# Optimization experiments

Hardware: AMD Instinct MI355X
Metric: run time of the kernel (lower is better)

## Reference

```python
import jax, jax.numpy as jnp
import numpy as np

S_SCALE = 64.0   # arcface scale
MARGIN = 0.5     # arcface additive angular margin
EMB = 512
NUM_CLASSES = 100000
BATCH = 512


def setup_inputs() -> dict:
    key = jax.random.key(0)
    k1, k2, k3, k4 = jax.random.split(key, 4)
    # xavier_uniform for [num_classes, emb]
    limit = float(np.sqrt(6.0 / (NUM_CLASSES + EMB)))
    weight = jax.random.uniform(k1, (NUM_CLASSES, EMB), jnp.float32, -limit, limit)
    fc_weight = jax.random.uniform(k2, (NUM_CLASSES, EMB), jnp.float32, -limit, limit)
    local_embeddings = jax.random.normal(k3, (BATCH, EMB), jnp.float32)
    local_labels = jax.random.randint(k4, (BATCH,), 0, NUM_CLASSES, jnp.int64)
    return {
        "local_embeddings": local_embeddings,
        "weight": weight,
        "fc_weight": fc_weight,
        "local_labels": local_labels,
        "epoch": 40,
    }


def _l2norm(x, eps=1e-12):
    return x / jnp.maximum(jnp.linalg.norm(x, axis=-1, keepdims=True), eps)


def _arcface(logits, labels):
    # insightface ArcFace: replace target cosine with cos(theta + m), then scale by s
    rows = jnp.arange(logits.shape[0])
    target = logits[rows, labels]
    sin = jnp.sqrt(jnp.maximum(1.0 - target * target, 0.0))
    cos_m, sin_m = jnp.cos(MARGIN), jnp.sin(MARGIN)
    with_margin = target * cos_m - sin * sin_m            # cos(theta + m)
    # safeguard: only apply when theta + m <= pi  (target > cos(pi - m))
    threshold = jnp.cos(jnp.pi - MARGIN)
    mm = jnp.sin(jnp.pi - MARGIN) * MARGIN
    new_target = jnp.where(target > threshold, with_margin, target - mm)
    logits = logits.at[rows, labels].set(new_target)
    return logits * S_SCALE


def _ce(logits, labels):
    rows = jnp.arange(logits.shape[0])
    logp = jax.nn.log_softmax(logits, axis=-1)
    return -jnp.mean(logp[rows, labels])


def reference(local_embeddings, weight, fc_weight, local_labels, epoch):
    labels = local_labels.astype(jnp.int32)
    # margin branch: normalize both sides, cosine logits, arcface margin, CE
    norm_emb = _l2norm(local_embeddings)
    norm_w = _l2norm(weight)
    logits = norm_emb @ norm_w.T                   # [B, num_classes]
    logits = _arcface(logits, labels)
    margin_loss = _ce(logits, labels)
    # plain CE branch on raw linear
    ce_logits = local_embeddings @ fc_weight.T     # [B, num_classes]
    ce_loss = _ce(ce_logits, labels)
    if epoch <= 30:
        return ce_loss + 0.0 * margin_loss
    else:
        return 0.0 * ce_loss + margin_loss
```

## Files before the change

kernel.cpp:

```cpp
#include <hip/hip_runtime.h>

typedef float floatx4 __attribute__((ext_vector_type(4)));
typedef int   intx4   __attribute__((ext_vector_type(4)));
typedef int   intx8   __attribute__((ext_vector_type(8)));

#define NC      100000
#define EMBD    512
#define BATCH   512
#define BN      64
#define NCH     1563
#define NGB     196

#define COS_M   0.8775825618903728f
#define SIN_M   0.479425538604203f
#define THRESH  (-0.8775825618903728f)
#define MM_C    0.2397127693021015f

__device__ __forceinline__ uint2 pack8_fp8(float4 a, float4 b) {
  int lo = 0, hi = 0;
  lo = __builtin_amdgcn_cvt_pk_fp8_f32(a.x, a.y, lo, false);
  lo = __builtin_amdgcn_cvt_pk_fp8_f32(a.z, a.w, lo, true);
  hi = __builtin_amdgcn_cvt_pk_fp8_f32(b.x, b.y, hi, false);
  hi = __builtin_amdgcn_cvt_pk_fp8_f32(b.z, b.w, hi, true);
  return make_uint2((unsigned)lo, (unsigned)hi);
}

__global__ __launch_bounds__(256) void prep_small_k(
    const float* __restrict__ emb, const float* __restrict__ weight,
    const float* __restrict__ fcw, const int* __restrict__ labels,
    const int* __restrict__ epoch, unsigned char* __restrict__ Aq,
    float* __restrict__ tsc, int* __restrict__ lab32,
    float* __restrict__ out) {
  const bool mm = (*epoch > 30);
  const int tid = threadIdx.x;
  const int pred = (labels[2 * tid + 1] != 0) ? 1 : 0;
  const bool is64 = (__syncthreads_or(pred) == 0);

  const int w = tid >> 6, lane = tid & 63;
  const int row = blockIdx.x * 4 + w;
  const int lab = is64 ? labels[2 * row] : labels[row];
  const float* W = mm ? weight : fcw;

  const float* er = emb + (size_t)row * EMBD + lane * 8;
  const float* wr = W + (size_t)lab * EMBD + lane * 8;
  float4 e0 = *(const float4*)er,  e1 = *(const float4*)(er + 4);
  float4 w0 = *(const float4*)wr,  w1 = *(const float4*)(wr + 4);
  float dot = e0.x*w0.x + e0.y*w0.y + e0.z*w0.z + e0.w*w0.w
            + e1.x*w1.x + e1.y*w1.y + e1.z*w1.z + e1.w*w1.w;
  float ssa = e0.x*e0.x + e0.y*e0.y + e0.z*e0.z + e0.w*e0.w
            + e1.x*e1.x + e1.y*e1.y + e1.z*e1.z + e1.w*e1.w;
  float ssw = w0.x*w0.x + w0.y*w0.y + w0.z*w0.z + w0.w*w0.w
            + w1.x*w1.x + w1.y*w1.y + w1.z*w1.z + w1.w*w1.w;
  #pragma unroll
  for (int off = 32; off; off >>= 1) {
    dot += __shfl_xor(dot, off, 64);
    ssa += __shfl_xor(ssa, off, 64);
    ssw += __shfl_xor(ssw, off, 64);
  }
  const float inva = mm ? (1.0f / fmaxf(sqrtf(ssa), 1e-12f)) : 1.0f;
  float4 q0 = make_float4(e0.x*inva, e0.y*inva, e0.z*inva, e0.w*inva);
  float4 q1 = make_float4(e1.x*inva, e1.y*inva, e1.z*inva, e1.w*inva);
  *(uint2*)(Aq + (size_t)row * EMBD + lane * 8) = pack8_fp8(q0, q1);

  if (lane == 0) {
    lab32[row] = lab;
    float tv;
    if (mm) {
      float cosv = dot / (fmaxf(sqrtf(ssa), 1e-12f) * fmaxf(sqrtf(ssw), 1e-12f));
      float sinv = sqrtf(fmaxf(1.0f - cosv * cosv, 0.0f));
      float wmarg = cosv * COS_M - sinv * SIN_M;
      float nt = (cosv > THRESH) ? wmarg : (cosv - MM_C);
      tv = 64.0f * nt;
    } else {
      tv = dot;
    }
    tsc[row] = tv;
  }
  if (blockIdx.x == 0 && tid == 0) out[0] = 0.0f;
}

__global__ __launch_bounds__(256, 2) void gemm_fused_k(
    const unsigned char* __restrict__ Aq, const float* __restrict__ weight,
    const float* __restrict__ fcw, const float* __restrict__ tsc,
    const int* __restrict__ lab32, const int* __restrict__ epoch,
    float2* __restrict__ partials) {
  const int t = blockIdx.x & 31, gblk = blockIdx.x >> 5;
  const int bn = gblk * 8 + (t & 7);
  const int bm = t >> 3;
  if (bn >= NCH) return;

  const bool mm = (*epoch > 30);
  const float scale = mm ? 64.0f : 1.0f;
  const float* __restrict__ Wp = mm ? weight : fcw;

  __shared__ unsigned char Bs[BN * EMBD];
  __shared__ float tscS[128];
  __shared__ int   labS[128];

  const int tid  = threadIdx.x;
  const int lane = tid & 63;
  const int w    = tid >> 6;
  const int m0   = bm * 128;
  const int n0   = bn * BN;

  if (tid < 128) { tscS[tid] = tsc[m0 + tid]; labS[tid] = lab32[m0 + tid]; }

  #pragma unroll 4
  for (int rr = 0; rr < 16; ++rr) {
    const int r    = w * 16 + rr;
    const int grow = n0 + r;
    uint2 pq = make_uint2(0u, 0u);
    if (grow < NC) {
      const float* src = Wp + (size_t)grow * EMBD + lane * 8;
      float4 a = *(const float4*)src;
      float4 b = *(const float4*)(src + 4);
      float ss = a.x*a.x + a.y*a.y + a.z*a.z + a.w*a.w
               + b.x*b.x + b.y*b.y + b.z*b.z + b.w*b.w;
      #pragma unroll
      for (int off = 32; off; off >>= 1) ss += __shfl_xor(ss, off, 64);
      const float inv = mm ? (1.0f / fmaxf(sqrtf(ss), 1e-12f)) : 1.0f;
      float4 qa = make_float4(a.x*inv, a.y*inv, a.z*inv, a.w*inv);
      float4 qb = make_float4(b.x*inv, b.y*inv, b.z*inv, b.w*inv);
      pq = pack8_fp8(qa, qb);
    }
    const int addr = r * EMBD + ((lane >> 4) << 7)
                   + (((((lane >> 1) & 7) ^ (r & 7))) << 4) + ((lane & 1) << 3);
    *(uint2*)&Bs[addr] = pq;
  }
  __syncthreads();

  const int rsel = lane & 15;
  const int g32  = (lane >> 4) * 32;
  const int c0   = ((((lane >> 4) * 2)     ^ (rsel & 7)) << 4);
  const int c1   = (((((lane >> 4) * 2)+1) ^ (rsel & 7)) << 4);

  floatx4 acc[2][4];
  #pragma unroll
  for (int i = 0; i < 2; i++)
    #pragma unroll
    for (int j = 0; j < 4; j++) acc[i][j] = (floatx4){0.f, 0.f, 0.f, 0.f};

  #pragma unroll
  for (int kt = 0; kt < 4; ++kt) {
    intx8 af[2];
    #pragma unroll
    for (int mi = 0; mi < 2; mi++) {
      const unsigned char* ap =
          Aq + (size_t)(m0 + w * 32 + mi * 16 + rsel) * EMBD + kt * 128 + g32;
      intx4 alo = *(const intx4*)ap;
      intx4 ahi = *(const intx4*)(ap + 16);
      af[mi] = __builtin_shufflevector(alo, ahi, 0, 1, 2, 3, 4, 5, 6, 7);
    }
    intx8 bv[4];
    #pragma unroll
    for (int ni = 0; ni < 4; ni++) {
      const int base = (ni * 16 + rsel) * EMBD + kt * 128;
      intx4 lo = *(const intx4*)&Bs[base + c0];
      intx4 hi = *(const intx4*)&Bs[base + c1];
      bv[ni] = __builtin_shufflevector(lo, hi, 0, 1, 2, 3, 4, 5, 6, 7);
    }
    #pragma unroll
    for (int mi = 0; mi < 2; mi++)
      #pragma unroll
      for (int ni = 0; ni < 4; ni++)
        acc[mi][ni] = __builtin_amdgcn_mfma_scale_f32_16x16x128_f8f6f4(
            af[mi], bv[ni], acc[mi][ni], 0, 0,
            0, 0x7f7f7f7f, 0, 0x7f7f7f7f);
  }

  const int colq = lane & 15;
  #pragma unroll
  for (int mi = 0; mi < 2; mi++) {
    #pragma unroll
    for (int r = 0; r < 4; r++) {
      const int rl = w * 32 + mi * 16 + (lane >> 4) * 4 + r;
      const int lab = labS[rl];
      const float tv = tscS[rl];
      float v[4];
      #pragma unroll
      for (int ni = 0; ni < 4; ni++) {
        const int cg = n0 + ni * 16 + colq;
        float x = acc[mi][ni][r] * scale;
        if (cg >= NC) x = -1e30f;
        else if (cg == lab) x = tv;
        v[ni] = x;
      }
      float mx = v[0];
      #pragma unroll
      for (int ni = 1; ni < 4; ni++) mx = fmaxf(mx, v[ni]);
      #pragma unroll
      for (int off = 1; off < 16; off <<= 1) mx = fmaxf(mx, __shfl_xor(mx, off, 64));
      float s = 0.0f;
      #pragma unroll
      for (int ni = 0; ni < 4; ni++) s += __expf(v[ni] - mx);
      #pragma unroll
      for (int off = 1; off < 16; off <<= 1) s += __shfl_xor(s, off, 64);
      if (colq == 0)
        partials[(size_t)(m0 + rl) * NCH + bn] = make_float2(mx, s);
    }
  }
}

__global__ __launch_bounds__(256) void rowmerge_k(
    const float2* __restrict__ partials, const float* __restrict__ tsc,
    float* __restrict__ out) {
  const int row = blockIdx.x;
  const int tid = threadIdx.x;
  float M = -1e30f, S = 0.0f;
  for (int j = tid; j < NCH; j += 256) {
    const float2 p = partials[(size_t)row * NCH + j];
    if (p.x > M) { S = S * __expf(M - p.x) + p.y; M = p.x; }
    else         { S += p.y * __expf(p.x - M); }
  }
  __shared__ float sm[256], sv[256];
  sm[tid] = M; sv[tid] = S;
  __syncthreads();
  for (int st = 128; st > 0; st >>= 1) {
    if (tid < st) {
      const float m2 = sm[tid + st], s2 = sv[tid + st];
      const float m1 = sm[tid],      s1 = sv[tid];
      const float Mn = fmaxf(m1, m2);
      sv[tid] = s1 * __expf(m1 - Mn) + s2 * __expf(m2 - Mn);
      sm[tid] = Mn;
    }
    __syncthreads();
  }
  if (tid == 0) {
    const float loss = (sm[0] + __logf(sv[0])) - tsc[row];
    atomicAdd(out, loss * (1.0f / 512.0f));
  }
}

extern "C" void kernel_launch(void* const* d_in, const int* in_sizes, int n_in,
                              void* d_out, int out_size, void* d_ws, size_t ws_size,
                              hipStream_t stream) {
  const float* emb    = (const float*)d_in[0];
  const float* weight = (const float*)d_in[1];
  const float* fcw    = (const float*)d_in[2];
  const int*   labels = (const int*)d_in[3];
  const int*   epoch  = (const int*)d_in[4];
  float* out = (float*)d_out;

  char* ws = (char*)d_ws;
  size_t off = 0;
  unsigned char* Aq = (unsigned char*)(ws + off); off += (size_t)BATCH * EMBD;
  float* tsc       = (float*)(ws + off); off += BATCH * 4;
  int* lab32       = (int*)(ws + off);   off += BATCH * 4;
  float2* partials = (float2*)(ws + off); off += (size_t)BATCH * NCH * 8;

  prep_small_k<<<BATCH / 4, 256, 0, stream>>>(emb, weight, fcw, labels, epoch,
                                              Aq, tsc, lab32, out);
  gemm_fused_k<<<NGB * 32, 256, 0, stream>>>(Aq, weight, fcw, tsc, lab32, epoch,
                                             partials);
  rowmerge_k<<<BATCH, 256, 0, stream>>>(partials, tsc, out);
}
```

Baseline: 564.5 us.

## Double M tile to 256 and defer weight-norm scaling to epilogue

New measurement: 507.9 us. -10.0%, faster.

```diff
diff --git a/kernel.cpp b/kernel.cpp
--- a/kernel.cpp
+++ b/kernel.cpp
@@ -8,8 +8,12 @@
 #define EMBD    512
 #define BATCH   512
 #define BN      64
+#define BM      256
 #define NCH     1563
 #define NGB     196
+
+#define WSCALE      1024.0f
+#define INV_WSCALE  (1.0f / 1024.0f)
 
 #define COS_M   0.8775825618903728f
 #define SIN_M   0.479425538604203f
@@ -84,7 +88,7 @@
     const float* __restrict__ fcw, const float* __restrict__ tsc,
     const int* __restrict__ lab32, const int* __restrict__ epoch,
     float2* __restrict__ partials) {
-  const int t = blockIdx.x & 31, gblk = blockIdx.x >> 5;
+  const int t = blockIdx.x & 15, gblk = blockIdx.x >> 4;
   const int bn = gblk * 8 + (t & 7);
   const int bm = t >> 3;
   if (bn >= NCH) return;
@@ -94,38 +98,55 @@
   const float* __restrict__ Wp = mm ? weight : fcw;
 
   __shared__ unsigned char Bs[BN * EMBD];
-  __shared__ float tscS[128];
-  __shared__ int   labS[128];
+  __shared__ float tscS[BM];
+  __shared__ int   labS[BM];
+  __shared__ float invnS[BN];
 
   const int tid  = threadIdx.x;
   const int lane = tid & 63;
   const int w    = tid >> 6;
-  const int m0   = bm * 128;
+  const int m0   = bm * BM;
   const int n0   = bn * BN;
 
-  if (tid < 128) { tscS[tid] = tsc[m0 + tid]; labS[tid] = lab32[m0 + tid]; }
-
-  #pragma unroll 4
+  tscS[tid] = tsc[m0 + tid];
+  labS[tid] = lab32[m0 + tid];
+
+  float ssp[16];
+  #pragma unroll
   for (int rr = 0; rr < 16; ++rr) {
     const int r    = w * 16 + rr;
     const int grow = n0 + r;
     uint2 pq = make_uint2(0u, 0u);
+    float ssl = 0.0f;
     if (grow < NC) {
       const float* src = Wp + (size_t)grow * EMBD + lane * 8;
       float4 a = *(const float4*)src;
       float4 b = *(const float4*)(src + 4);
-      float ss = a.x*a.x + a.y*a.y + a.z*a.z + a.w*a.w
-               + b.x*b.x + b.y*b.y + b.z*b.z + b.w*b.w;
-      #pragma unroll
-      for (int off = 32; off; off >>= 1) ss += __shfl_xor(ss, off, 64);
-      const float inv = mm ? (1.0f / fmaxf(sqrtf(ss), 1e-12f)) : 1.0f;
-      float4 qa = make_float4(a.x*inv, a.y*inv, a.z*inv, a.w*inv);
-      float4 qb = make_float4(b.x*inv, b.y*inv, b.z*inv, b.w*inv);
+      ssl = a.x*a.x + a.y*a.y + a.z*a.z + a.w*a.w
+          + b.x*b.x + b.y*b.y + b.z*b.z + b.w*b.w;
+      float4 qa = make_float4(a.x*WSCALE, a.y*WSCALE, a.z*WSCALE, a.w*WSCALE);
+      float4 qb = make_float4(b.x*WSCALE, b.y*WSCALE, b.z*WSCALE, b.w*WSCALE);
       pq = pack8_fp8(qa, qb);
     }
+    ssp[rr] = ssl;
     const int addr = r * EMBD + ((lane >> 4) << 7)
                    + (((((lane >> 1) & 7) ^ (r & 7))) << 4) + ((lane & 1) << 3);
     *(uint2*)&Bs[addr] = pq;
+  }
+
+  #pragma unroll
+  for (int rr = 0; rr < 16; ++rr) {
+    float s = ssp[rr];
+    #pragma unroll
+    for (int off = 32; off; off >>= 1) s += __shfl_xor(s, off, 64);
+    ssp[rr] = s;
+  }
+  if (lane == 0) {
+    #pragma unroll
+    for (int rr = 0; rr < 16; ++rr) {
+      invnS[w * 16 + rr] =
+          mm ? (INV_WSCALE / fmaxf(sqrtf(ssp[rr]), 1e-12f)) : INV_WSCALE;
+    }
   }
   __syncthreads();
 
@@ -134,19 +155,19 @@
   const int c0   = ((((lane >> 4) * 2)     ^ (rsel & 7)) << 4);
   const int c1   = (((((lane >> 4) * 2)+1) ^ (rsel & 7)) << 4);
 
-  floatx4 acc[2][4];
-  #pragma unroll
-  for (int i = 0; i < 2; i++)
+  floatx4 acc[4][4];
+  #pragma unroll
+  for (int i = 0; i < 4; i++)
     #pragma unroll
     for (int j = 0; j < 4; j++) acc[i][j] = (floatx4){0.f, 0.f, 0.f, 0.f};
 
   #pragma unroll
   for (int kt = 0; kt < 4; ++kt) {
-    intx8 af[2];
-    #pragma unroll
-    for (int mi = 0; mi < 2; mi++) {
+    intx8 af[4];
+    #pragma unroll
+    for (int mi = 0; mi < 4; mi++) {
       const unsigned char* ap =
-          Aq + (size_t)(m0 + w * 32 + mi * 16 + rsel) * EMBD + kt * 128 + g32;
+          Aq + (size_t)(m0 + w * 64 + mi * 16 + rsel) * EMBD + kt * 128 + g32;
       intx4 alo = *(const intx4*)ap;
       intx4 ahi = *(const intx4*)(ap + 16);
       af[mi] = __builtin_shufflevector(alo, ahi, 0, 1, 2, 3, 4, 5, 6, 7);
@@ -160,7 +181,7 @@
       bv[ni] = __builtin_shufflevector(lo, hi, 0, 1, 2, 3, 4, 5, 6, 7);
     }
     #pragma unroll
-    for (int mi = 0; mi < 2; mi++)
+    for (int mi = 0; mi < 4; mi++)
       #pragma unroll
       for (int ni = 0; ni < 4; ni++)
         acc[mi][ni] = __builtin_amdgcn_mfma_scale_f32_16x16x128_f8f6f4(
@@ -170,17 +191,17 @@
 
   const int colq = lane & 15;
   #pragma unroll
-  for (int mi = 0; mi < 2; mi++) {
+  for (int mi = 0; mi < 4; mi++) {
     #pragma unroll
     for (int r = 0; r < 4; r++) {
-      const int rl = w * 32 + mi * 16 + (lane >> 4) * 4 + r;
+      const int rl = w * 64 + mi * 16 + (lane >> 4) * 4 + r;
       const int lab = labS[rl];
       const float tv = tscS[rl];
       float v[4];
       #pragma unroll
       for (int ni = 0; ni < 4; ni++) {
         const int cg = n0 + ni * 16 + colq;
-        float x = acc[mi][ni][r] * scale;
+        float x = acc[mi][ni][r] * scale * invnS[ni * 16 + colq];
         if (cg >= NC) x = -1e30f;
         else if (cg == lab) x = tv;
         v[ni] = x;
@@ -250,7 +271,7 @@
 
   prep_small_k<<<BATCH / 4, 256, 0, stream>>>(emb, weight, fcw, labels, epoch,
                                               Aq, tsc, lab32, out);
-  gemm_fused_k<<<NGB * 32, 256, 0, stream>>>(Aq, weight, fcw, tsc, lab32, epoch,
+  gemm_fused_k<<<NGB * 16, 256, 0, stream>>>(Aq, weight, fcw, tsc, lab32, epoch,
                                              partials);
   rowmerge_k<<<BATCH, 256, 0, stream>>>(partials, tsc, out);
 }
```
